# Kernel tuning notes

Hardware: AMD Instinct MI355X
Metric: run time of the kernel (lower is better)

The kernel has to match this reference:

```python
import jax, jax.numpy as jnp
import numpy as np

B, L, D = 2048, 64, 300   # batch, words per sentence, embedding dim (== kernel_size)
C = 512                    # conv out_channels
H, O = 2048, 1             # fc hidden, fc output


def setup_inputs() -> dict:
    key = jax.random.key(0)
    ks = jax.random.split(key, 8)
    s = 0.05
    return {
        "x1": jax.random.normal(ks[0], (B, L, D), jnp.float32),
        "x2": jax.random.normal(ks[1], (B, L, D), jnp.float32),
        # Conv1d(in=1, out=C, kernel=D) weight is [C,1,D]; stored as [C,D]
        "Wc": jax.random.normal(ks[2], (C, D), jnp.float32) * s,
        "bc": jax.random.normal(ks[3], (C,), jnp.float32) * s,
        "W1": jax.random.normal(ks[4], (H, 2 * C), jnp.float32) * s,
        "b1": jax.random.normal(ks[5], (H,), jnp.float32) * s,
        "W2": jax.random.normal(ks[6], (O, H), jnp.float32) * s,
        "b2": jax.random.normal(ks[7], (O,), jnp.float32) * s,
    }


def reference(x1, x2, Wc, bc, W1, b1, W2, b2):
    # Per-word Conv1d(kernel=D) + ReLU is a full-width filter == linear map D->C.
    # Batch all words in one einsum instead of the original Python loop.
    def encode(x):
        h = jax.nn.relu(jnp.einsum('bld,cd->blc', x, Wc) + bc)  # [B,L,C]
        return jnp.max(h, axis=1)                                # max over words -> [B,C]

    e1 = encode(x1)
    e2 = encode(x2)
    feat = jnp.concatenate([e1 - e2, e1 * e2], axis=1)           # [B,2C]
    h = jnp.tanh(feat @ W1.T + b1)                               # [B,H]
    return h @ W2.T + b2                                         # [B,O]
```

## Files before the change

kernel.cpp:

```cpp
#include <hip/hip_runtime.h>


#define B_SZ 2048
#define L_SZ 64
#define D_SZ 300
#define C_SZ 512
#define H_SZ 2048
#define KPAD 320
#define NKC 40
#define LDSPITCH 328

typedef __bf16 bf16x8 __attribute__((ext_vector_type(8)));
typedef float f32x4 __attribute__((ext_vector_type(4)));

__device__ __forceinline__ unsigned short f2bf(float f) {
  unsigned int u = __float_as_uint(f);
  u += 0x7fffu + ((u >> 16) & 1u);
  return (unsigned short)(u >> 16);
}

__global__ __launch_bounds__(256)
void convert_kernel(const float* __restrict__ Wc, const float* __restrict__ W1,
                    unsigned short* __restrict__ WcSwz, unsigned short* __restrict__ W1Swz) {
  int id = blockIdx.x * 256 + threadIdx.x;
  if (id < C_SZ * NKC) {
    int c = id / NKC, kc = id - c * NKC;
    unsigned short tmp[8];
    #pragma unroll
    for (int i = 0; i < 8; ++i) {
      int k = kc * 8 + i;
      tmp[i] = (k < D_SZ) ? f2bf(Wc[c * D_SZ + k]) : (unsigned short)0;
    }
    unsigned short* dst = WcSwz + (((c >> 4) * NKC + kc) * 16 + (c & 15)) * 8;
    *reinterpret_cast<uint4*>(dst) = *reinterpret_cast<uint4*>(tmp);
    return;
  }
  id -= C_SZ * NKC;
  if (id < H_SZ * 128) {
    int j = id >> 7, kc = id & 127;
    const float* src = W1 + (size_t)j * 1024 + kc * 8;
    unsigned short tmp[8];
    #pragma unroll
    for (int i = 0; i < 8; ++i) tmp[i] = f2bf(src[i]);
    unsigned short* dst = W1Swz + (((j >> 4) * 128 + kc) * 16 + (j & 15)) * 8;
    *reinterpret_cast<uint4*>(dst) = *reinterpret_cast<uint4*>(tmp);
  }
}

__global__ __launch_bounds__(256)
void encode_kernel(const float* __restrict__ x1, const float* __restrict__ x2,
                   const unsigned short* __restrict__ WcSwz,
                   const float* __restrict__ bc, float* __restrict__ e) {
  const int b = blockIdx.x, z = blockIdx.y;
  const float* __restrict__ x = (z ? x2 : x1) + (size_t)b * (L_SZ * D_SZ);
  __shared__ unsigned short xs[L_SZ * LDSPITCH];
  const int tid = threadIdx.x;

  const float4* __restrict__ xv = reinterpret_cast<const float4*>(x);
  for (int i = tid; i < (L_SZ * D_SZ / 4); i += 256) {
    float4 v = xv[i];
    int word = i / 75, col = (i - word * 75) * 4;
    unsigned int lo = (unsigned int)f2bf(v.x) | ((unsigned int)f2bf(v.y) << 16);
    unsigned int hi = (unsigned int)f2bf(v.z) | ((unsigned int)f2bf(v.w) << 16);
    *reinterpret_cast<uint2*>(&xs[word * LDSPITCH + col]) = make_uint2(lo, hi);
  }
  for (int i = tid; i < L_SZ * (KPAD - D_SZ); i += 256) {
    int word = i / 20, c = D_SZ + (i - word * 20);
    xs[word * LDSPITCH + c] = 0;
  }
  __syncthreads();

  const int wave = tid >> 6, lane = tid & 63;
  const int l16 = lane & 15, quad = lane >> 4;
  const int koff = quad * 8;

  f32x4 acc[4][8];
  #pragma unroll
  for (int mt = 0; mt < 4; ++mt)
    #pragma unroll
    for (int nt = 0; nt < 8; ++nt)
      #pragma unroll
      for (int r = 0; r < 4; ++r) acc[mt][nt][r] = 0.f;

  #pragma unroll
  for (int ks = 0; ks < KPAD / 32; ++ks) {
    bf16x8 a[4];
    #pragma unroll
    for (int mt = 0; mt < 4; ++mt)
      a[mt] = *reinterpret_cast<const bf16x8*>(&xs[(mt * 16 + l16) * LDSPITCH + ks * 32 + koff]);
    #pragma unroll
    for (int nt = 0; nt < 8; ++nt) {
      const unsigned short* bp =
          WcSwz + ((((wave * 8 + nt) * NKC) + ks * 4 + quad) * 16 + l16) * 8;
      bf16x8 bw = *reinterpret_cast<const bf16x8*>(bp);
      #pragma unroll
      for (int mt = 0; mt < 4; ++mt)
        acc[mt][nt] = __builtin_amdgcn_mfma_f32_16x16x32_bf16(a[mt], bw, acc[mt][nt], 0, 0, 0);
    }
  }

  #pragma unroll
  for (int nt = 0; nt < 8; ++nt) {
    int c = wave * 128 + nt * 16 + l16;
    float bias = bc[c];
    float v = 0.f;
    #pragma unroll
    for (int mt = 0; mt < 4; ++mt)
      #pragma unroll
      for (int r = 0; r < 4; ++r)
        v = fmaxf(v, acc[mt][nt][r] + bias);
    v = fmaxf(v, __shfl_xor(v, 16));
    v = fmaxf(v, __shfl_xor(v, 32));
    if (quad == 0)
      e[((size_t)z * B_SZ + b) * C_SZ + c] = v;
  }
}

__global__ __launch_bounds__(256)
void feat_kernel(const float* __restrict__ e, unsigned short* __restrict__ featSwz) {
  int id = blockIdx.x * 256 + threadIdx.x;
  if (id >= B_SZ * 128) return;
  int b = id >> 7, kc = id & 127;
  unsigned short tmp[8];
  #pragma unroll
  for (int i = 0; i < 8; ++i) {
    int k = kc * 8 + i, c = k & 511;
    float a = e[(size_t)b * C_SZ + c];
    float bb = e[(size_t)B_SZ * C_SZ + (size_t)b * C_SZ + c];
    tmp[i] = f2bf((k < C_SZ) ? (a - bb) : (a * bb));
  }
  unsigned short* dst = featSwz + (((b >> 4) * 128 + kc) * 16 + (b & 15)) * 8;
  *reinterpret_cast<uint4*>(dst) = *reinterpret_cast<uint4*>(tmp);
}

__global__ __launch_bounds__(256, 4)
void fc1_kernel(const unsigned short* __restrict__ featSwz,
                const unsigned short* __restrict__ W1Swz,
                const float* __restrict__ b1, const float* __restrict__ W2,
                float* __restrict__ partial) {
  const int mbase = blockIdx.x * 32;
  const int tid = threadIdx.x;
  const int wave = tid >> 6, lane = tid & 63;
  const int l16 = lane & 15, quad = lane >> 4;
  const int nbase = blockIdx.y * 128 + wave * 32;

  f32x4 acc[2][2];
  #pragma unroll
  for (int mt = 0; mt < 2; ++mt)
    #pragma unroll
    for (int nt = 0; nt < 2; ++nt)
      #pragma unroll
      for (int r = 0; r < 4; ++r) acc[mt][nt][r] = 0.f;

  #pragma unroll 4
  for (int ks = 0; ks < 32; ++ks) {
    bf16x8 a[2], bw[2];
    #pragma unroll
    for (int mt = 0; mt < 2; ++mt)
      a[mt] = *reinterpret_cast<const bf16x8*>(
          featSwz + (((size_t)(blockIdx.x * 2 + mt) * 128 + ks * 4 + quad) * 16 + l16) * 8);
    #pragma unroll
    for (int nt = 0; nt < 2; ++nt)
      bw[nt] = *reinterpret_cast<const bf16x8*>(
          W1Swz + (((size_t)(blockIdx.y * 8 + wave * 2 + nt) * 128 + ks * 4 + quad) * 16 + l16) * 8);
    #pragma unroll
    for (int mt = 0; mt < 2; ++mt)
      #pragma unroll
      for (int nt = 0; nt < 2; ++nt)
        acc[mt][nt] = __builtin_amdgcn_mfma_f32_16x16x32_bf16(a[mt], bw[nt], acc[mt][nt], 0, 0, 0);
  }

  float c[2][4];
  #pragma unroll
  for (int mt = 0; mt < 2; ++mt)
    #pragma unroll
    for (int r = 0; r < 4; ++r) c[mt][r] = 0.f;

  #pragma unroll
  for (int nt = 0; nt < 2; ++nt) {
    int j = nbase + nt * 16 + l16;
    float bias = b1[j];
    float w2 = W2[j];
    #pragma unroll
    for (int mt = 0; mt < 2; ++mt)
      #pragma unroll
      for (int r = 0; r < 4; ++r) {
        float pre = acc[mt][nt][r] + bias;
        pre = fminf(fmaxf(pre, -15.f), 15.f);
        float ex = __expf(2.f * pre);
        c[mt][r] += w2 * ((ex - 1.f) / (ex + 1.f));
      }
  }
  #pragma unroll
  for (int off = 1; off <= 8; off <<= 1)
    #pragma unroll
    for (int mt = 0; mt < 2; ++mt)
      #pragma unroll
      for (int r = 0; r < 4; ++r)
        c[mt][r] += __shfl_xor(c[mt][r], off);

  if (l16 == 0) {
    int slice = blockIdx.y * 4 + wave;
    #pragma unroll
    for (int mt = 0; mt < 2; ++mt)
      #pragma unroll
      for (int r = 0; r < 4; ++r) {
        int brow = mbase + mt * 16 + quad * 4 + r;
        partial[(size_t)slice * B_SZ + brow] = c[mt][r];
      }
  }
}

__global__ __launch_bounds__(256)
void finalize_kernel(const float* __restrict__ partial, const float* __restrict__ b2,
                     float* __restrict__ out) {
  int b = blockIdx.x * 256 + threadIdx.x;
  float s = b2[0];
  #pragma unroll 8
  for (int i = 0; i < 64; ++i) s += partial[(size_t)i * B_SZ + b];
  out[b] = s;
}

extern "C" void kernel_launch(void* const* d_in, const int* in_sizes, int n_in,
                              void* d_out, int out_size, void* d_ws, size_t ws_size,
                              hipStream_t stream) {
  const float* x1 = (const float*)d_in[0];
  const float* x2 = (const float*)d_in[1];
  const float* Wc = (const float*)d_in[2];
  const float* bc = (const float*)d_in[3];
  const float* W1 = (const float*)d_in[4];
  const float* b1 = (const float*)d_in[5];
  const float* W2 = (const float*)d_in[6];
  const float* b2 = (const float*)d_in[7];

  char* ws = (char*)d_ws;
  unsigned short* WcSwz   = (unsigned short*)(ws);
  unsigned short* W1Swz   = (unsigned short*)(ws + 327680);
  float*          e       = (float*)(ws + 4521984);
  unsigned short* featSwz = (unsigned short*)(ws + 12910592);
  float*          partial = (float*)(ws + 17104896);

  {
    int total = C_SZ * NKC + H_SZ * 128;
    convert_kernel<<<(total + 255) / 256, 256, 0, stream>>>(Wc, W1, WcSwz, W1Swz);
  }
  encode_kernel<<<dim3(B_SZ, 2), 256, 0, stream>>>(x1, x2, WcSwz, bc, e);
  feat_kernel<<<(B_SZ * 128 + 255) / 256, 256, 0, stream>>>(e, featSwz);
  fc1_kernel<<<dim3(B_SZ / 32, H_SZ / 128), 256, 0, stream>>>(featSwz, W1Swz, b1, W2, partial);
  finalize_kernel<<<B_SZ / 256, 256, 0, stream>>>(partial, b2, (float*)d_out);
}
```

Before: 489.2 us.

## Load encode A-operands directly from global memory, bypassing LDS staging

The encode kernel no longer stages each sentence into shared memory as bf16 with a barrier. Each lane now reads its MFMA A-fragments straight from global fp32 rows and converts them in registers, zero-filling the K tail past 300. The change also adds a min-blocks hint of 2 to launch_bounds. This removes the LDS writes, the padding loop and the __syncthreads. In exchange every wave reloads the same x rows from global or L2, four times per block, using row-strided float4 loads with partial coalescing, and register pressure may rise.

```diff
diff --git a/kernel.cpp b/kernel.cpp
--- a/kernel.cpp
+++ b/kernel.cpp
@@ -6,9 +6,7 @@
 #define D_SZ 300
 #define C_SZ 512
 #define H_SZ 2048
-#define KPAD 320
 #define NKC 40
-#define LDSPITCH 328
 
 typedef __bf16 bf16x8 __attribute__((ext_vector_type(8)));
 typedef float f32x4 __attribute__((ext_vector_type(4)));
@@ -17,6 +15,13 @@
   unsigned int u = __float_as_uint(f);
   u += 0x7fffu + ((u >> 16) & 1u);
   return (unsigned short)(u >> 16);
+}
+
+__device__ __forceinline__ bf16x8 cvt8(float4 v0, float4 v1) {
+  bf16x8 r;
+  r[0] = (__bf16)v0.x; r[1] = (__bf16)v0.y; r[2] = (__bf16)v0.z; r[3] = (__bf16)v0.w;
+  r[4] = (__bf16)v1.x; r[5] = (__bf16)v1.y; r[6] = (__bf16)v1.z; r[7] = (__bf16)v1.w;
+  return r;
 }
 
 __global__ __launch_bounds__(256)
@@ -47,32 +52,20 @@
   }
 }
 
-__global__ __launch_bounds__(256)
+__global__ __launch_bounds__(256, 2)
 void encode_kernel(const float* __restrict__ x1, const float* __restrict__ x2,
                    const unsigned short* __restrict__ WcSwz,
                    const float* __restrict__ bc, float* __restrict__ e) {
   const int b = blockIdx.x, z = blockIdx.y;
   const float* __restrict__ x = (z ? x2 : x1) + (size_t)b * (L_SZ * D_SZ);
-  __shared__ unsigned short xs[L_SZ * LDSPITCH];
   const int tid = threadIdx.x;
-
-  const float4* __restrict__ xv = reinterpret_cast<const float4*>(x);
-  for (int i = tid; i < (L_SZ * D_SZ / 4); i += 256) {
-    float4 v = xv[i];
-    int word = i / 75, col = (i - word * 75) * 4;
-    unsigned int lo = (unsigned int)f2bf(v.x) | ((unsigned int)f2bf(v.y) << 16);
-    unsigned int hi = (unsigned int)f2bf(v.z) | ((unsigned int)f2bf(v.w) << 16);
-    *reinterpret_cast<uint2*>(&xs[word * LDSPITCH + col]) = make_uint2(lo, hi);
-  }
-  for (int i = tid; i < L_SZ * (KPAD - D_SZ); i += 256) {
-    int word = i / 20, c = D_SZ + (i - word * 20);
-    xs[word * LDSPITCH + c] = 0;
-  }
-  __syncthreads();
-
   const int wave = tid >> 6, lane = tid & 63;
   const int l16 = lane & 15, quad = lane >> 4;
-  const int koff = quad * 8;
+
+  const float* rowp[4];
+  #pragma unroll
+  for (int mt = 0; mt < 4; ++mt)
+    rowp[mt] = x + (mt * 16 + l16) * D_SZ + quad * 8;
 
   f32x4 acc[4][8];
   #pragma unroll
@@ -83,11 +76,22 @@
       for (int r = 0; r < 4; ++r) acc[mt][nt][r] = 0.f;
 
   #pragma unroll
-  for (int ks = 0; ks < KPAD / 32; ++ks) {
+  for (int ks = 0; ks < 10; ++ks) {
     bf16x8 a[4];
     #pragma unroll
-    for (int mt = 0; mt < 4; ++mt)
-      a[mt] = *reinterpret_cast<const bf16x8*>(&xs[(mt * 16 + l16) * LDSPITCH + ks * 32 + koff]);
+    for (int mt = 0; mt < 4; ++mt) {
+      float4 v0, v1;
+      if (ks < 9) {
+        v0 = *reinterpret_cast<const float4*>(rowp[mt] + ks * 32);
+        v1 = *reinterpret_cast<const float4*>(rowp[mt] + ks * 32 + 4);
+      } else {
+        v0 = make_float4(0.f, 0.f, 0.f, 0.f);
+        v1 = v0;
+        if (quad < 2)  v0 = *reinterpret_cast<const float4*>(rowp[mt] + 288);
+        if (quad == 0) v1 = *reinterpret_cast<const float4*>(rowp[mt] + 292);
+      }
+      a[mt] = cvt8(v0, v1);
+    }
     #pragma unroll
     for (int nt = 0; nt < 8; ++nt) {
       const unsigned short* bp =
```

New measurement: 515.8 us. 5.4% more time.
